# Kernel optimization log

Hardware: AMD Instinct MI355X
Metric: run time of the kernel (lower is better)

The kernel has to match this reference:

```python
import jax, jax.numpy as jnp
import numpy as np


def setup_inputs() -> dict:
    key = jax.random.key(0)
    ks = jax.random.split(key, 6)
    B, F, E, H, U = 64, 4096, 256, 512, 512
    scale = 0.02
    return {
        "features": jax.random.normal(ks[0], (B, F, E), dtype=jnp.float32),
        "hidden": jax.random.normal(ks[1], (B, H), dtype=jnp.float32),
        "W1_w": jax.random.normal(ks[2], (E, U), dtype=jnp.float32) * scale,
        "W1_b": jnp.zeros((U,), dtype=jnp.float32),
        "W2_w": jax.random.normal(ks[3], (H, U), dtype=jnp.float32) * scale,
        "W2_b": jnp.zeros((U,), dtype=jnp.float32),
        "V_w": jax.random.normal(ks[4], (U, 1), dtype=jnp.float32) * scale,
        "V_b": jnp.zeros((1,), dtype=jnp.float32),
    }


def reference(features, hidden, W1_w, W1_b, W2_w, W2_b, V_w, V_b):
    # features: (B, F, E); hidden: (B, H)
    proj_f = jnp.einsum("bfe,eu->bfu", features, W1_w) + W1_b          # (B, F, U)
    proj_h = (hidden @ W2_w + W2_b)[:, None, :]                        # (B, 1, U)
    attention_hidden = jnp.tanh(proj_f + proj_h)                       # (B, F, U)
    scores = jnp.einsum("bfu,uo->bfo", attention_hidden, V_w) + V_b    # (B, F, 1)
    attention_weights = jax.nn.softmax(scores, axis=1)                 # (B, F, 1)
    context_vector = jnp.sum(attention_weights * features, axis=1)     # (B, E)
    return (context_vector, attention_weights)
```

## Files before the change

kernel.cpp:

```cpp
#include <hip/hip_runtime.h>
#include <cmath>

constexpr int Bdim = 64;
constexpr int Fdim = 4096;
constexpr int Edim = 256;
constexpr int Hdim = 512;
constexpr int Udim = 512;

typedef __attribute__((ext_vector_type(8))) short short8;
typedef __attribute__((ext_vector_type(4))) float f32x4;

__device__ __forceinline__ unsigned short f2bf(float f) {
    unsigned int u = __float_as_uint(f);
    u += 0x7FFFu + ((u >> 16) & 1u);
    return (unsigned short)(u >> 16);
}
__device__ __forceinline__ unsigned int pack2(float lo, float hi) {
    return (unsigned int)f2bf(lo) | ((unsigned int)f2bf(hi) << 16);
}
__device__ __forceinline__ float tanh_fast(float x) {
    float e = __expf(2.0f * x);
    return 1.0f - 2.0f * __builtin_amdgcn_rcpf(e + 1.0f);
}
__device__ __forceinline__ void gload_lds16(const void* g, void* l) {
    __builtin_amdgcn_global_load_lds(
        (const __attribute__((address_space(1))) unsigned int*)g,
        (__attribute__((address_space(3))) unsigned int*)l, 16, 0, 0);
}

__global__ __launch_bounds__(256) void proj_h_kernel(
    const float* __restrict__ hidden, const float* __restrict__ W2,
    const float* __restrict__ W1b, const float* __restrict__ W2b,
    float* __restrict__ cb)
{
    const int b = blockIdx.x;
    const int u = blockIdx.y * 256 + threadIdx.x;
    const float* hb = hidden + (size_t)b * Hdim;
    float acc = 0.f;
    #pragma unroll 8
    for (int h = 0; h < Hdim; ++h)
        acc = fmaf(hb[h], W2[(size_t)h * Udim + u], acc);
    cb[(size_t)b * Udim + u] = acc + W1b[u] + W2b[u];
}

__global__ __launch_bounds__(256) void w1t_kernel(
    const float* __restrict__ W1, unsigned short* __restrict__ Th)
{
    __shared__ unsigned short sT[64][72];
    const int e0 = blockIdx.x * 64, u0 = blockIdx.y * 64;
    const int tid = threadIdx.x;
    const int ue = tid & 63, er = tid >> 6;
    #pragma unroll
    for (int it = 0; it < 16; ++it) {
        const int e = er + it * 4;
        sT[ue][e] = f2bf(W1[(size_t)(e0 + e) * Udim + u0 + ue]);
    }
    __syncthreads();
    const int ur = tid >> 2, cq = tid & 3;
    const int u = u0 + ur, s = u & 7;
    const int cA = (e0 >> 3) + cq * 2;
    uint4 a  = *(const uint4*)&sT[ur][cq * 16];
    uint4 b2 = *(const uint4*)&sT[ur][cq * 16 + 8];
    unsigned short* dst = Th + (size_t)u * Edim;
    *(uint4*)(dst + ((cA ^ s) << 3))       = a;
    *(uint4*)(dst + (((cA + 1) ^ s) << 3)) = b2;
}

__global__ __launch_bounds__(256, 2) void score_mfma4_kernel(
    const float* __restrict__ feat,
    const unsigned short* __restrict__ W1Ts,
    const float* __restrict__ Vw, const float* __restrict__ Vb,
    const float* __restrict__ cb, float* __restrict__ scores)
{
    __shared__ unsigned short lds[16896];

    const int b    = blockIdx.y;
    const int f0   = blockIdx.x * 128;
    const int tid  = threadIdx.x;
    const int lane = tid & 63;
    const int w    = tid >> 6;
    const int ln15 = lane & 15;
    const int kq   = lane >> 4;
    const int swz  = ln15 & 7;

    short8 af[2][8];
    {
        unsigned short* sAw = lds + w * 4224;
        const float* gA = feat + ((size_t)(b * Fdim + f0 + w * 32)) * Edim;
        #pragma unroll
        for (int h = 0; h < 2; ++h) {
            #pragma unroll
            for (int r = 0; r < 16; ++r) {
                float4 v = *(const float4*)(gA + (size_t)(h * 16 + r) * Edim + lane * 4);
                uint2 p; p.x = pack2(v.x, v.y); p.y = pack2(v.z, v.w);
                *(uint2*)&sAw[r * 264 + lane * 4] = p;
            }
            #pragma unroll
            for (int k8 = 0; k8 < 8; ++k8)
                af[h][k8] = *(const short8*)&sAw[ln15 * 264 + k8 * 32 + kq * 8];
        }
    }
    __syncthreads();

    float sacc[2][4] = {};
    const float* cbB = cb + (size_t)b * Udim;

    for (int up = 0; up < 8; ++up) {
        if (up) __syncthreads();
        const char* gB = (const char*)(W1Ts + (size_t)up * 64 * Edim);
        #pragma unroll
        for (int t = 0; t < 8; ++t) {
            const int chunk = w * 8 + t;
            gload_lds16(gB + (size_t)chunk * 1024 + lane * 16,
                        (char*)lds + chunk * 1024);
        }
        __syncthreads();

        #pragma unroll
        for (int sp = 0; sp < 2; ++sp) {
            const int ub = up * 64 + sp * 32;
            const float cu0 = cbB[ub + ln15],     cu1 = cbB[ub + 16 + ln15];
            const float vv0 = Vw[ub + ln15],      vv1 = Vw[ub + 16 + ln15];
            f32x4 acc[2][2] = {};
            #pragma unroll
            for (int k8 = 0; k8 < 8; ++k8) {
                const int co = ((k8 * 4 + kq) ^ swz) * 8;
                short8 b0 = *(const short8*)&lds[(sp * 32 + ln15) * 256 + co];
                short8 b1 = *(const short8*)&lds[(sp * 32 + 16 + ln15) * 256 + co];
                #pragma unroll
                for (int mi = 0; mi < 2; ++mi) {
                    acc[mi][0] = __builtin_amdgcn_mfma_f32_16x16x32_bf16(
                        af[mi][k8], b0, acc[mi][0], 0, 0, 0);
                    acc[mi][1] = __builtin_amdgcn_mfma_f32_16x16x32_bf16(
                        af[mi][k8], b1, acc[mi][1], 0, 0, 0);
                }
            }
            #pragma unroll
            for (int mi = 0; mi < 2; ++mi)
                #pragma unroll
                for (int r = 0; r < 4; ++r)
                    sacc[mi][r] += tanh_fast(acc[mi][0][r] + cu0) * vv0
                                 + tanh_fast(acc[mi][1][r] + cu1) * vv1;
        }
    }

    const float vb = Vb[0];
    #pragma unroll
    for (int mi = 0; mi < 2; ++mi)
        #pragma unroll
        for (int r = 0; r < 4; ++r) {
            float s = sacc[mi][r];
            s += __shfl_xor(s, 1);
            s += __shfl_xor(s, 2);
            s += __shfl_xor(s, 4);
            s += __shfl_xor(s, 8);
            if (ln15 == 0)
                scores[(size_t)b * Fdim + f0 + w * 32 + mi * 16 + kq * 4 + r] = s + vb;
        }
}

constexpr int TFt = 64;
constexpr int TUt = 64;
constexpr int LDR = Edim + 4;

__global__ __launch_bounds__(256) void score_kernel(
    const float* __restrict__ feat, const float* __restrict__ W1,
    const float* __restrict__ Vw, const float* __restrict__ Vb,
    const float* __restrict__ cb, float* __restrict__ scores)
{
    __shared__ float sA[TFt * LDR];
    __shared__ float sW[TUt * LDR];

    const int b   = blockIdx.y;
    const int f0  = blockIdx.x * TFt;
    const int tid = threadIdx.x;
    const int tf  = tid >> 4;
    const int tu  = tid & 15;

    {
        const float4* gA = (const float4*)(feat + ((size_t)b * Fdim + f0) * Edim);
        #pragma unroll
        for (int it = 0; it < 16; ++it) {
            const int i = tid + it * 256;
            const int f = i >> 6;
            const int qq = i & 63;
            const float4 v = gA[i];
            *(float4*)&sA[f * LDR + 4 * qq] = v;
        }
    }

    float sacc[4] = {0.f, 0.f, 0.f, 0.f};
    const float* cbb = cb + (size_t)b * Udim;

    for (int uc = 0; uc < Udim; uc += TUt) {
        __syncthreads();
        #pragma unroll
        for (int it = 0; it < 16; ++it) {
            const int i = tid + it * 256;
            const int e = i >> 4;
            const int qq = i & 15;
            const float4 v = *(const float4*)(W1 + (size_t)e * Udim + uc + 4 * qq);
            sW[(4 * qq + 0) * LDR + e] = v.x;
            sW[(4 * qq + 1) * LDR + e] = v.y;
            sW[(4 * qq + 2) * LDR + e] = v.z;
            sW[(4 * qq + 3) * LDR + e] = v.w;
        }
        __syncthreads();

        float acc[4][4] = {};
        #pragma unroll 4
        for (int e = 0; e < Edim; e += 4) {
            float4 a0 = *(const float4*)&sA[(tf +  0) * LDR + e];
            float4 a1 = *(const float4*)&sA[(tf + 16) * LDR + e];
            float4 a2 = *(const float4*)&sA[(tf + 32) * LDR + e];
            float4 a3 = *(const float4*)&sA[(tf + 48) * LDR + e];
            float4 w0 = *(const float4*)&sW[(tu +  0) * LDR + e];
            float4 w1 = *(const float4*)&sW[(tu + 16) * LDR + e];
            float4 w2 = *(const float4*)&sW[(tu + 32) * LDR + e];
            float4 w3 = *(const float4*)&sW[(tu + 48) * LDR + e];
            #define FMA4(i, j, A, W)                         \
                acc[i][j] = fmaf(A.x, W.x, acc[i][j]);       \
                acc[i][j] = fmaf(A.y, W.y, acc[i][j]);       \
                acc[i][j] = fmaf(A.z, W.z, acc[i][j]);       \
                acc[i][j] = fmaf(A.w, W.w, acc[i][j]);
            FMA4(0,0,a0,w0) FMA4(0,1,a0,w1) FMA4(0,2,a0,w2) FMA4(0,3,a0,w3)
            FMA4(1,0,a1,w0) FMA4(1,1,a1,w1) FMA4(1,2,a1,w2) FMA4(1,3,a1,w3)
            FMA4(2,0,a2,w0) FMA4(2,1,a2,w1) FMA4(2,2,a2,w2) FMA4(2,3,a2,w3)
            FMA4(3,0,a3,w0) FMA4(3,1,a3,w1) FMA4(3,2,a3,w2) FMA4(3,3,a3,w3)
            #undef FMA4
        }

        #pragma unroll
        for (int j = 0; j < 4; ++j) {
            const int u = uc + tu + 16 * j;
            const float vw = Vw[u];
            const float cuv = cbb[u];
            #pragma unroll
            for (int i = 0; i < 4; ++i)
                sacc[i] = fmaf(tanhf(acc[i][j] + cuv), vw, sacc[i]);
        }
    }

    const float vb = Vb[0];
    #pragma unroll
    for (int i = 0; i < 4; ++i) {
        float s = sacc[i];
        s += __shfl_xor(s, 1);
        s += __shfl_xor(s, 2);
        s += __shfl_xor(s, 4);
        s += __shfl_xor(s, 8);
        if (tu == 0)
            scores[(size_t)b * Fdim + f0 + tf + 16 * i] = s + vb;
    }
}

__global__ __launch_bounds__(256) void softmax_kernel(float* __restrict__ sc)
{
    __shared__ float red[256];
    const int b = blockIdx.x;
    const int tid = threadIdx.x;
    float* row = sc + (size_t)b * Fdim;

    float v[16];
    float m = -INFINITY;
    #pragma unroll
    for (int i = 0; i < 16; ++i) {
        v[i] = row[tid + 256 * i];
        m = fmaxf(m, v[i]);
    }
    red[tid] = m;
    __syncthreads();
    for (int s = 128; s > 0; s >>= 1) {
        if (tid < s) red[tid] = fmaxf(red[tid], red[tid + s]);
        __syncthreads();
    }
    m = red[0];
    __syncthreads();

    float sum = 0.f;
    #pragma unroll
    for (int i = 0; i < 16; ++i) {
        v[i] = expf(v[i] - m);
        sum += v[i];
    }
    red[tid] = sum;
    __syncthreads();
    for (int s = 128; s > 0; s >>= 1) {
        if (tid < s) red[tid] += red[tid + s];
        __syncthreads();
    }
    const float inv = 1.f / red[0];
    #pragma unroll
    for (int i = 0; i < 16; ++i)
        row[tid + 256 * i] = v[i] * inv;
}

__global__ __launch_bounds__(256) void context_kernel(
    const float* __restrict__ feat, const float* __restrict__ wts,
    float* __restrict__ ctx)
{
    const int b  = blockIdx.y;
    const int fc = blockIdx.x;
    const int e  = threadIdx.x;

    const float* fp = feat + ((size_t)b * Fdim + (size_t)fc * 256) * Edim + e;
    const float* wp = wts + (size_t)b * Fdim + (size_t)fc * 256;

    float acc = 0.f;
    #pragma unroll 8
    for (int f = 0; f < 256; ++f)
        acc = fmaf(wp[f], fp[(size_t)f * Edim], acc);

    atomicAdd(&ctx[(size_t)b * Edim + e], acc);
}

extern "C" void kernel_launch(void* const* d_in, const int* in_sizes, int n_in,
                              void* d_out, int out_size, void* d_ws, size_t ws_size,
                              hipStream_t stream)
{
    const float* features = (const float*)d_in[0];
    const float* hidden   = (const float*)d_in[1];
    const float* W1w      = (const float*)d_in[2];
    const float* W1b      = (const float*)d_in[3];
    const float* W2w      = (const float*)d_in[4];
    const float* W2b      = (const float*)d_in[5];
    const float* Vw       = (const float*)d_in[6];
    const float* Vb       = (const float*)d_in[7];

    float* ctx = (float*)d_out;
    float* wts = (float*)d_out + (size_t)Bdim * Edim;

    float* cb = (float*)d_ws;
    unsigned short* W1Ts = (unsigned short*)((char*)d_ws + 131072);
    const size_t NEED = 131072 + (size_t)Udim * Edim * 2;

    hipMemsetAsync(ctx, 0, (size_t)Bdim * Edim * sizeof(float), stream);
    dim3 pgrid(Bdim, Udim / 256);
    proj_h_kernel<<<pgrid, 256, 0, stream>>>(hidden, W2w, W1b, W2b, cb);

    if (ws_size >= NEED) {
        dim3 tgrid(Edim / 64, Udim / 64);
        w1t_kernel<<<tgrid, 256, 0, stream>>>(W1w, W1Ts);
        dim3 sgrid(Fdim / 128, Bdim);
        score_mfma4_kernel<<<sgrid, 256, 0, stream>>>(features, W1Ts, Vw, Vb, cb, wts);
    } else {
        dim3 sgrid(Fdim / TFt, Bdim);
        score_kernel<<<sgrid, 256, 0, stream>>>(features, W1w, Vw, Vb, cb, wts);
    }

    softmax_kernel<<<Bdim, 256, 0, stream>>>(wts);

    dim3 cgrid(16, Bdim);
    context_kernel<<<cgrid, 256, 0, stream>>>(features, wts, ctx);
}
```

Before: 490.0 us.

## Merge prep kernels, double-buffer W1 tiles, fuse softmax normalize into context

Folds the hidden projection, W1 transpose and ctx zeroing into a single prep launch, which removes the memset and one kernel launch. The score kernel now streams W1 in 32-column tiles into double-buffered LDS, so the next tile loads while the current one feeds the MFMAs. Softmax is split into a stats pass using wave-shuffle reductions and a fused pass that normalizes weights while computing the context with float4 loads. The trade-off is more launches' worth of logic in fewer kernels, a different LDS footprint that could affect occupancy, and some scores recomputed through expf in the context pass.

Measured after the change: 480.4 us. -2.0%, faster.

```diff
diff --git a/kernel.cpp b/kernel.cpp
--- a/kernel.cpp
+++ b/kernel.cpp
@@ -28,42 +28,49 @@
         (__attribute__((address_space(3))) unsigned int*)l, 16, 0, 0);
 }
 
-__global__ __launch_bounds__(256) void proj_h_kernel(
+__global__ __launch_bounds__(256) void prep_kernel(
     const float* __restrict__ hidden, const float* __restrict__ W2,
     const float* __restrict__ W1b, const float* __restrict__ W2b,
-    float* __restrict__ cb)
-{
-    const int b = blockIdx.x;
-    const int u = blockIdx.y * 256 + threadIdx.x;
-    const float* hb = hidden + (size_t)b * Hdim;
-    float acc = 0.f;
-    #pragma unroll 8
-    for (int h = 0; h < Hdim; ++h)
-        acc = fmaf(hb[h], W2[(size_t)h * Udim + u], acc);
-    cb[(size_t)b * Udim + u] = acc + W1b[u] + W2b[u];
-}
-
-__global__ __launch_bounds__(256) void w1t_kernel(
-    const float* __restrict__ W1, unsigned short* __restrict__ Th)
-{
-    __shared__ unsigned short sT[64][72];
-    const int e0 = blockIdx.x * 64, u0 = blockIdx.y * 64;
+    float* __restrict__ cb,
+    const float* __restrict__ W1, unsigned short* __restrict__ Th,
+    float* __restrict__ ctx, const int do_t)
+{
+    const int bid = blockIdx.x;
     const int tid = threadIdx.x;
-    const int ue = tid & 63, er = tid >> 6;
-    #pragma unroll
-    for (int it = 0; it < 16; ++it) {
-        const int e = er + it * 4;
-        sT[ue][e] = f2bf(W1[(size_t)(e0 + e) * Udim + u0 + ue]);
-    }
-    __syncthreads();
-    const int ur = tid >> 2, cq = tid & 3;
-    const int u = u0 + ur, s = u & 7;
-    const int cA = (e0 >> 3) + cq * 2;
-    uint4 a  = *(const uint4*)&sT[ur][cq * 16];
-    uint4 b2 = *(const uint4*)&sT[ur][cq * 16 + 8];
-    unsigned short* dst = Th + (size_t)u * Edim;
-    *(uint4*)(dst + ((cA ^ s) << 3))       = a;
-    *(uint4*)(dst + (((cA + 1) ^ s) << 3)) = b2;
+
+    if (bid < 128) {
+        const int b = bid >> 1;
+        const int u = (bid & 1) * 256 + tid;
+        const float* hb = hidden + (size_t)b * Hdim;
+        float acc = 0.f;
+        #pragma unroll 8
+        for (int h = 0; h < Hdim; ++h)
+            acc = fmaf(hb[h], W2[(size_t)h * Udim + u], acc);
+        cb[(size_t)b * Udim + u] = acc + W1b[u] + W2b[u];
+    } else if (bid < 160) {
+        if (!do_t) return;
+        __shared__ unsigned short sT[64][72];
+        const int k  = bid - 128;
+        const int e0 = (k & 3) * 64, u0 = (k >> 2) * 64;
+        const int ue = tid & 63, er = tid >> 6;
+        #pragma unroll
+        for (int it = 0; it < 16; ++it) {
+            const int e = er + it * 4;
+            sT[ue][e] = f2bf(W1[(size_t)(e0 + e) * Udim + u0 + ue]);
+        }
+        __syncthreads();
+        const int ur = tid >> 2, cq = tid & 3;
+        const int u = u0 + ur, s = u & 7;
+        const int cA = (e0 >> 3) + cq * 2;
+        uint4 a  = *(const uint4*)&sT[ur][cq * 16];
+        uint4 b2 = *(const uint4*)&sT[ur][cq * 16 + 8];
+        unsigned short* dst = Th + (size_t)u * Edim;
+        *(uint4*)(dst + ((cA ^ s) << 3))       = a;
+        *(uint4*)(dst + (((cA + 1) ^ s) << 3)) = b2;
+    } else {
+        const int idx = (bid - 160) * 256 + tid;
+        ((float4*)ctx)[idx] = make_float4(0.f, 0.f, 0.f, 0.f);
+    }
 }
 
 __global__ __launch_bounds__(256, 2) void score_mfma4_kernel(
@@ -105,43 +112,55 @@
     float sacc[2][4] = {};
     const float* cbB = cb + (size_t)b * Udim;
 
-    for (int up = 0; up < 8; ++up) {
-        if (up) __syncthreads();
-        const char* gB = (const char*)(W1Ts + (size_t)up * 64 * Edim);
-        #pragma unroll
-        for (int t = 0; t < 8; ++t) {
-            const int chunk = w * 8 + t;
+    {
+        const char* gB = (const char*)W1Ts;
+        #pragma unroll
+        for (int t = 0; t < 4; ++t) {
+            const int chunk = w * 4 + t;
             gload_lds16(gB + (size_t)chunk * 1024 + lane * 16,
                         (char*)lds + chunk * 1024);
         }
-        __syncthreads();
-
-        #pragma unroll
-        for (int sp = 0; sp < 2; ++sp) {
-            const int ub = up * 64 + sp * 32;
-            const float cu0 = cbB[ub + ln15],     cu1 = cbB[ub + 16 + ln15];
-            const float vv0 = Vw[ub + ln15],      vv1 = Vw[ub + 16 + ln15];
-            f32x4 acc[2][2] = {};
-            #pragma unroll
-            for (int k8 = 0; k8 < 8; ++k8) {
-                const int co = ((k8 * 4 + kq) ^ swz) * 8;
-                short8 b0 = *(const short8*)&lds[(sp * 32 + ln15) * 256 + co];
-                short8 b1 = *(const short8*)&lds[(sp * 32 + 16 + ln15) * 256 + co];
-                #pragma unroll
-                for (int mi = 0; mi < 2; ++mi) {
-                    acc[mi][0] = __builtin_amdgcn_mfma_f32_16x16x32_bf16(
-                        af[mi][k8], b0, acc[mi][0], 0, 0, 0);
-                    acc[mi][1] = __builtin_amdgcn_mfma_f32_16x16x32_bf16(
-                        af[mi][k8], b1, acc[mi][1], 0, 0, 0);
-                }
+    }
+    __syncthreads();
+
+    for (int p = 0; p < 16; ++p) {
+        if (p < 15) {
+            const char* gB = (const char*)(W1Ts + (size_t)(p + 1) * 32 * Edim);
+            char* lb = (char*)lds + ((p + 1) & 1) * 16384;
+            #pragma unroll
+            for (int t = 0; t < 4; ++t) {
+                const int chunk = w * 4 + t;
+                gload_lds16(gB + (size_t)chunk * 1024 + lane * 16,
+                            lb + chunk * 1024);
             }
-            #pragma unroll
-            for (int mi = 0; mi < 2; ++mi)
-                #pragma unroll
-                for (int r = 0; r < 4; ++r)
-                    sacc[mi][r] += tanh_fast(acc[mi][0][r] + cu0) * vv0
-                                 + tanh_fast(acc[mi][1][r] + cu1) * vv1;
-        }
+        }
+
+        const unsigned short* bw = lds + (p & 1) * 8192;
+        const int ub = p * 32;
+        const float cu0 = cbB[ub + ln15],     cu1 = cbB[ub + 16 + ln15];
+        const float vv0 = Vw[ub + ln15],      vv1 = Vw[ub + 16 + ln15];
+        f32x4 acc[2][2] = {};
+        #pragma unroll
+        for (int k8 = 0; k8 < 8; ++k8) {
+            const int co = ((k8 * 4 + kq) ^ swz) * 8;
+            short8 b0 = *(const short8*)&bw[ln15 * 256 + co];
+            short8 b1 = *(const short8*)&bw[(16 + ln15) * 256 + co];
+            #pragma unroll
+            for (int mi = 0; mi < 2; ++mi) {
+                acc[mi][0] = __builtin_amdgcn_mfma_f32_16x16x32_bf16(
+                    af[mi][k8], b0, acc[mi][0], 0, 0, 0);
+                acc[mi][1] = __builtin_amdgcn_mfma_f32_16x16x32_bf16(
+                    af[mi][k8], b1, acc[mi][1], 0, 0, 0);
+            }
+        }
+        #pragma unroll
+        for (int mi = 0; mi < 2; ++mi)
+            #pragma unroll
+            for (int r = 0; r < 4; ++r)
+                sacc[mi][r] += tanh_fast(acc[mi][0][r] + cu0) * vv0
+                             + tanh_fast(acc[mi][1][r] + cu1) * vv1;
+
+        if (p < 15) __syncthreads();
     }
 
     const float vb = Vb[0];
@@ -254,12 +273,13 @@
     }
 }
 
-__global__ __launch_bounds__(256) void softmax_kernel(float* __restrict__ sc)
-{
-    __shared__ float red[256];
-    const int b = blockIdx.x;
+__global__ __launch_bounds__(256) void softmax_stats_kernel(
+    const float* __restrict__ sc, float2* __restrict__ st)
+{
+    __shared__ float red[8];
+    const int b   = blockIdx.x;
     const int tid = threadIdx.x;
-    float* row = sc + (size_t)b * Fdim;
+    const float* row = sc + (size_t)b * Fdim;
 
     float v[16];
     float m = -INFINITY;
@@ -268,50 +288,75 @@
         v[i] = row[tid + 256 * i];
         m = fmaxf(m, v[i]);
     }
-    red[tid] = m;
-    __syncthreads();
-    for (int s = 128; s > 0; s >>= 1) {
-        if (tid < s) red[tid] = fmaxf(red[tid], red[tid + s]);
-        __syncthreads();
-    }
-    m = red[0];
-    __syncthreads();
-
-    float sum = 0.f;
-    #pragma unroll
-    for (int i = 0; i < 16; ++i) {
-        v[i] = expf(v[i] - m);
-        sum += v[i];
-    }
-    red[tid] = sum;
-    __syncthreads();
-    for (int s = 128; s > 0; s >>= 1) {
-        if (tid < s) red[tid] += red[tid + s];
-        __syncthreads();
-    }
-    const float inv = 1.f / red[0];
+    #pragma unroll
+    for (int off = 1; off < 64; off <<= 1)
+        m = fmaxf(m, __shfl_xor(m, off));
+    if ((tid & 63) == 0) red[tid >> 6] = m;
+    __syncthreads();
+    m = fmaxf(fmaxf(red[0], red[1]), fmaxf(red[2], red[3]));
+
+    float s = 0.f;
     #pragma unroll
     for (int i = 0; i < 16; ++i)
-        row[tid + 256 * i] = v[i] * inv;
-}
-
-__global__ __launch_bounds__(256) void context_kernel(
-    const float* __restrict__ feat, const float* __restrict__ wts,
-    float* __restrict__ ctx)
-{
-    const int b  = blockIdx.y;
-    const int fc = blockIdx.x;
-    const int e  = threadIdx.x;
-
-    const float* fp = feat + ((size_t)b * Fdim + (size_t)fc * 256) * Edim + e;
-    const float* wp = wts + (size_t)b * Fdim + (size_t)fc * 256;
-
-    float acc = 0.f;
+        s += expf(v[i] - m);
+    #pragma unroll
+    for (int off = 1; off < 64; off <<= 1)
+        s += __shfl_xor(s, off);
+    if ((tid & 63) == 0) red[4 + (tid >> 6)] = s;
+    __syncthreads();
+    if (tid == 0) {
+        const float tot = red[4] + red[5] + red[6] + red[7];
+        st[b] = make_float2(m, 1.0f / tot);
+    }
+}
+
+__global__ __launch_bounds__(256) void ctxnorm_kernel(
+    const float* __restrict__ feat, const float2* __restrict__ st,
+    float* __restrict__ wts, float* __restrict__ ctx)
+{
+    __shared__ float  wl[256];
+    __shared__ float4 sred[256];
+
+    const int b   = blockIdx.y;
+    const int f0  = blockIdx.x * 256;
+    const int tid = threadIdx.x;
+
+    const float2 s2 = st[b];
+    const size_t wix = (size_t)b * Fdim + f0 + tid;
+    const float wgt = expf(wts[wix] - s2.x) * s2.y;
+    wts[wix] = wgt;
+    wl[tid]  = wgt;
+    __syncthreads();
+
+    const int e4 = tid & 63;
+    const int fg = tid >> 6;
+    const float4* fp = (const float4*)(feat + ((size_t)b * Fdim + f0) * Edim);
+
+    float4 a = make_float4(0.f, 0.f, 0.f, 0.f);
     #pragma unroll 8
-    for (int f = 0; f < 256; ++f)
-        acc = fmaf(wp[f], fp[(size_t)f * Edim], acc);
-
-    atomicAdd(&ctx[(size_t)b * Edim + e], acc);
+    for (int i = 0; i < 64; ++i) {
+        const int f = i * 4 + fg;
+        const float4 v = fp[(size_t)f * 64 + e4];
+        const float wv = wl[f];
+        a.x = fmaf(wv, v.x, a.x);
+        a.y = fmaf(wv, v.y, a.y);
+        a.z = fmaf(wv, v.z, a.z);
+        a.w = fmaf(wv, v.w, a.w);
+    }
+    sred[tid] = a;
+    __syncthreads();
+
+    if (fg == 0) {
+        const float4 r0 = sred[e4];
+        const float4 r1 = sred[64 + e4];
+        const float4 r2 = sred[128 + e4];
+        const float4 r3 = sred[192 + e4];
+        float* cp = ctx + (size_t)b * Edim + e4 * 4;
+        atomicAdd(cp + 0, r0.x + r1.x + r2.x + r3.x);
+        atomicAdd(cp + 1, r0.y + r1.y + r2.y + r3.y);
+        atomicAdd(cp + 2, r0.z + r1.z + r2.z + r3.z);
+        atomicAdd(cp + 3, r0.w + r1.w + r2.w + r3.w);
+    }
 }
 
 extern "C" void kernel_launch(void* const* d_in, const int* in_sizes, int n_in,
@@ -330,17 +375,16 @@
     float* ctx = (float*)d_out;
     float* wts = (float*)d_out + (size_t)Bdim * Edim;
 
-    float* cb = (float*)d_ws;
-    unsigned short* W1Ts = (unsigned short*)((char*)d_ws + 131072);
-    const size_t NEED = 131072 + (size_t)Udim * Edim * 2;
-
-    hipMemsetAsync(ctx, 0, (size_t)Bdim * Edim * sizeof(float), stream);
-    dim3 pgrid(Bdim, Udim / 256);
-    proj_h_kernel<<<pgrid, 256, 0, stream>>>(hidden, W2w, W1b, W2b, cb);
-
-    if (ws_size >= NEED) {
-        dim3 tgrid(Edim / 64, Udim / 64);
-        w1t_kernel<<<tgrid, 256, 0, stream>>>(W1w, W1Ts);
+    float*  cb    = (float*)d_ws;
+    float2* stats = (float2*)((char*)d_ws + 131072);
+    unsigned short* W1Ts = (unsigned short*)((char*)d_ws + 131584);
+    const size_t NEED = 131584 + (size_t)Udim * Edim * 2;
+    const int mfma_ok = (ws_size >= NEED) ? 1 : 0;
+
+    prep_kernel<<<176, 256, 0, stream>>>(hidden, W2w, W1b, W2b, cb,
+                                         W1w, W1Ts, ctx, mfma_ok);
+
+    if (mfma_ok) {
         dim3 sgrid(Fdim / 128, Bdim);
         score_mfma4_kernel<<<sgrid, 256, 0, stream>>>(features, W1Ts, Vw, Vb, cb, wts);
     } else {
@@ -348,8 +392,8 @@
         score_kernel<<<sgrid, 256, 0, stream>>>(features, W1w, Vw, Vb, cb, wts);
     }
 
-    softmax_kernel<<<Bdim, 256, 0, stream>>>(wts);
-
-    dim3 cgrid(16, Bdim);
-    context_kernel<<<cgrid, 256, 0, stream>>>(features, wts, ctx);
-}
+    softmax_stats_kernel<<<Bdim, 256, 0, stream>>>(wts, stats);
+
+    dim3 cgrid(Fdim / 256, Bdim);
+    ctxnorm_kernel<<<cgrid, 256, 0, stream>>>(features, stats, wts, ctx);
+}
```
